# Kernel tuning notes

Measured on AMD Instinct MI355X. Metric: run time of the kernel, lower is better.

The kernel has to match this reference:

```python
import jax, jax.numpy as jnp
import numpy as np

H, D, K, FF = 8, 512, 64, 64  # n_head, feature_dim, key_feature_dim, dim_feedforward
L, B = 512, 32
LN_EPS = 1e-5


def _l2norm(x, eps=1e-12):
    # torch F.normalize: x / max(||x||, eps)
    n = jnp.sqrt(jnp.sum(x * x, axis=-1, keepdims=True))
    return x / jnp.maximum(n, eps)


def _layernorm(x, g, b, eps=LN_EPS):
    m = jnp.mean(x, axis=-1, keepdims=True)
    v = jnp.mean((x - m) ** 2, axis=-1, keepdims=True)
    return (x - m) * jax.lax.rsqrt(v + eps) * g + b


def setup_inputs() -> dict:
    key0 = jax.random.key(0)
    ks = jax.random.split(key0, 13)
    n = jax.random.normal
    s_kq = float(np.sqrt(2.0 / K))
    s_v = float(np.sqrt(2.0 / D))
    return {
        "query": n(ks[0], (L, B, D), jnp.float32),
        "key": n(ks[1], (L, B, D), jnp.float32),
        "value": n(ks[2], (L, B, D), jnp.float32),
        "WK": n(ks[3], (H, K, D), jnp.float32) * s_kq,
        "WQ": n(ks[4], (H, K, D), jnp.float32) * s_kq,
        "WV": n(ks[5], (H, D, D), jnp.float32) * s_v,
        "Wt": n(ks[6], (H, D, D), jnp.float32) * 0.04,  # trans_conv (default kaiming-ish scale)
        "W1": n(ks[7], (H, FF, D), jnp.float32) * 0.04,
        "b1": jnp.zeros((H, FF), jnp.float32),
        "W2": n(ks[8], (H, D, FF), jnp.float32) * 0.1,
        "b2": jnp.zeros((H, D), jnp.float32),
        "ln_g": jnp.ones((H, D), jnp.float32),
        "ln_b": jnp.zeros((H, D), jnp.float32),
    }


def reference(query, key, value, WK, WQ, WV, Wt, W1, b1, W2, b2, ln_g, ln_b):
    # query/key/value: [L, B, D]; per-head weights stacked on leading H axis.
    Lq, Bb, Dd = query.shape
    Hh = WK.shape[0]

    # per-head cosine-normalized Q/K projections: [H, B, L, K]
    wq = _l2norm(jnp.einsum('lbd,hkd->hblk', query, WQ))
    wk = _l2norm(jnp.einsum('lbd,hkd->hblk', key, WK))

    # attention scores [H, B, Lq, Lk], temp = 1
    dot = jnp.einsum('hbqc,hbkc->hbqk', wq, wk)
    aff = jax.nn.softmax(dot, axis=-1)
    # custom renorm: divide by column sums over the QUERY axis
    aff = aff / (1e-9 + jnp.sum(aff, axis=2, keepdims=True))

    wv = jnp.einsum('lbd,hed->hble', value, WV)        # [H, B, Lk, D]
    out = jnp.einsum('hbqk,hbke->hbqe', aff, wv)       # [H, B, Lq, D]
    out = jnp.transpose(out, (0, 2, 1, 3))             # [H, L, B, D]

    # residual-style trans_conv(query - out) -> relu
    o = jax.nn.relu(jnp.einsum('hlbd,hed->hlbe', query[None] - out, Wt))

    # TransNonlinear FFN (dropout = identity at eval)
    hff = jax.nn.relu(jnp.einsum('hlbd,hfd->hlbf', o, W1) + b1[:, None, None, :])
    s2 = jnp.einsum('hlbf,hdf->hlbd', hff, W2) + b2[:, None, None, :]
    x = _layernorm(o + s2, ln_g[:, None, None, :], ln_b[:, None, None, :])

    # concat heads on last dim, head 0 first: [L, B, H*D]
    return jnp.transpose(x, (1, 2, 0, 3)).reshape(Lq, Bb, Hh * Dd)
```

## Files before the change

### kernel.cpp

```cpp
#include <hip/hip_runtime.h>
#include <stdint.h>

#define HH 8
#define DDIM 512
#define KHEAD 64
#define FFD 64
#define LLEN 512
#define BBATCH 32
#define NTOK 16384

typedef unsigned short u16;
typedef __attribute__((ext_vector_type(8))) __bf16 bf16x8;
typedef __attribute__((ext_vector_type(4))) float f32x4;

__device__ __forceinline__ float bf2f(u16 u) {
    union { uint32_t i; float f; } v; v.i = ((uint32_t)u) << 16; return v.f;
}
__device__ __forceinline__ u16 f2bf(float f) {
    union { uint32_t i; float f; } v; v.f = f;
    return (u16)((v.i + 0x7FFFu + ((v.i >> 16) & 1u)) >> 16);
}

__device__ __forceinline__ void gload16(const void* g, void* l) {
    __builtin_amdgcn_global_load_lds(
        (const __attribute__((address_space(1))) void*)g,
        (__attribute__((address_space(3))) void*)l, 16, 0, 0);
}

__global__ __launch_bounds__(256) void f2bf4(const float* __restrict__ in,
                                             u16* __restrict__ out, int n4) {
    int i = blockIdx.x * 256 + threadIdx.x;
    if (i >= n4) return;
    float4 v = ((const float4*)in)[i];
    ushort4 o; o.x = f2bf(v.x); o.y = f2bf(v.y); o.z = f2bf(v.z); o.w = f2bf(v.w);
    ((ushort4*)out)[i] = o;
}

enum { M_PLAIN = 0, M_WQK = 1, M_SUBAUX = 2, M_RELU = 3, M_ADDAUX = 4, M_SCALECOL = 5 };

template<int BM, int BN, int MODE, int ZMAP, int SWAPXY>
__global__ __launch_bounds__(256) void mgemm(
    const u16* __restrict__ A, const u16* __restrict__ B, u16* __restrict__ C,
    int Kd, int lda, int ldb, int ldc,
    long Ash, long Asb, long Bsh, long Bsb, long Csh, long Csb, int nB2,
    const float* __restrict__ bias, int biasN,
    const void* __restrict__ auxp, long auxsh, long auxsb, int auxld)
{
    constexpr int WC = (BN == 128) ? 2 : 1;
    constexpr int WR = 4 / WC;
    constexpr int WTM = BM / WR;
    constexpr int WTN = BN / WC;
    constexpr int MF = WTM / 16;
    constexpr int NF = WTN / 16;
    constexpr int NCA = (BM * 64) / 4096;
    constexpr int NCB = (BN * 64) / 4096;
    __shared__ u16 As[2][BM * 32];
    __shared__ u16 Bs[2][BN * 32];

    const int z = blockIdx.z;
    int h2, b2;
    if (ZMAP == 0)      { h2 = z / nB2;      b2 = z % nB2; }
    else if (ZMAP == 1) { h2 = z & 7;        b2 = z >> 3; }
    else                { h2 = (z >> 3) & 7; b2 = ((z >> 6) << 3) | (z & 7); }
    const u16* Ab = A + h2 * Ash + b2 * Asb;
    const u16* Bb = B + h2 * Bsh + b2 * Bsb;
    const int bx = SWAPXY ? blockIdx.y : blockIdx.x;
    const int by = SWAPXY ? blockIdx.x : blockIdx.y;
    const int m0 = bx * BM, n0 = by * BN;
    const int t = threadIdx.x;
    const int lane = t & 63;
    const int w = t >> 6;
    const int wr = w / WC, wc = w % WC;
    const int tb = t * 16;
    const int wb = (t & 192) * 16;

    f32x4 acc[MF][NF];
    #pragma unroll
    for (int m = 0; m < MF; ++m)
        #pragma unroll
        for (int n = 0; n < NF; ++n)
            #pragma unroll
            for (int i = 0; i < 4; ++i) acc[m][n][i] = 0.f;

    const int ko = (lane >> 4) * 16;

    auto stage = [&](int buf, int k0) {
        #pragma unroll
        for (int c = 0; c < NCA; ++c) {
            const int byte = c * 4096 + tb;
            const int row = byte >> 6;
            gload16((const char*)(Ab + (long)(m0 + row) * lda + k0) + (byte & 63),
                    (char*)As[buf] + c * 4096 + wb);
        }
        #pragma unroll
        for (int c = 0; c < NCB; ++c) {
            const int byte = c * 4096 + tb;
            const int row = byte >> 6;
            gload16((const char*)(Bb + (long)(n0 + row) * ldb + k0) + (byte & 63),
                    (char*)Bs[buf] + c * 4096 + wb);
        }
    };

    stage(0, 0);
    __syncthreads();
    int cur = 0;
    const int nsteps = Kd >> 5;
    for (int s = 0; s < nsteps; ++s) {
        if (s + 1 < nsteps) stage(cur ^ 1, (s + 1) << 5);
        bf16x8 af[MF], bfr[NF];
        #pragma unroll
        for (int m = 0; m < MF; ++m)
            af[m] = *(const bf16x8*)((const char*)As[cur] + (wr * WTM + m * 16 + (lane & 15)) * 64 + ko);
        #pragma unroll
        for (int n = 0; n < NF; ++n)
            bfr[n] = *(const bf16x8*)((const char*)Bs[cur] + (wc * WTN + n * 16 + (lane & 15)) * 64 + ko);
        #pragma unroll
        for (int m = 0; m < MF; ++m)
            #pragma unroll
            for (int n = 0; n < NF; ++n)
                acc[m][n] = __builtin_amdgcn_mfma_f32_16x16x32_bf16(af[m], bfr[n], acc[m][n], 0, 0, 0);
        __syncthreads();
        cur ^= 1;
    }

    const int lr = (lane >> 4) * 4;
    const int lc = lane & 15;

    if constexpr (MODE == M_WQK) {
        const int h = (n0 + wc * WTN) >> 6;
        #pragma unroll
        for (int m = 0; m < MF; ++m) {
            #pragma unroll
            for (int i = 0; i < 4; ++i) {
                float s = 0.f;
                #pragma unroll
                for (int n = 0; n < NF; ++n) { const float v = acc[m][n][i]; s += v * v; }
                s += __shfl_xor(s, 1); s += __shfl_xor(s, 2);
                s += __shfl_xor(s, 4); s += __shfl_xor(s, 8);
                const float inv = 1.0f / fmaxf(sqrtf(s), 1e-12f);
                const int r = m0 + wr * WTM + m * 16 + lr + i;
                const int l = r >> 5, bq = r & 31;
                const int sw = (l & 7) << 3;
                u16* rowp = C + (((long)(h * BBATCH + bq) * LLEN + l) * KHEAD);
                #pragma unroll
                for (int n = 0; n < NF; ++n)
                    rowp[(lc + n * 16) ^ sw] = f2bf(acc[m][n][i] * inv);
            }
        }
    } else {
        const long cof = h2 * Csh + b2 * Csb;
        #pragma unroll
        for (int m = 0; m < MF; ++m) {
            #pragma unroll
            for (int i = 0; i < 4; ++i) {
                const int r = m0 + wr * WTM + m * 16 + lr + i;
                #pragma unroll
                for (int n = 0; n < NF; ++n) {
                    const int c = n0 + wc * WTN + n * 16 + lc;
                    float v = acc[m][n][i];
                    if (MODE == M_SUBAUX) {
                        const u16* q = (const u16*)auxp;
                        v = bf2f(q[auxsh * h2 + auxsb * b2 + (long)r * auxld + c]) - v;
                    } else if (MODE == M_RELU) {
                        if (bias) v += bias[h2 * biasN + c];
                        v = fmaxf(v, 0.0f);
                    } else if (MODE == M_ADDAUX) {
                        v += bias[h2 * biasN + c];
                        const u16* ax = (const u16*)auxp;
                        v += bf2f(ax[auxsh * h2 + auxsb * b2 + (long)r * auxld + c]);
                    } else if (MODE == M_SCALECOL) {
                        const float* cs = (const float*)auxp + auxsh * h2 + auxsb * b2;
                        v *= 1.0f / (1e-9f + cs[c]);
                    }
                    C[cof + (long)r * ldc + c] = f2bf(v);
                }
            }
        }
    }
}

__global__ __launch_bounds__(256) void attn_mfma(
    const u16* __restrict__ wq, const u16* __restrict__ wk,
    u16* __restrict__ P, float* __restrict__ colsum)
{
    __shared__ u16 qs[64 * 64];
    __shared__ u16 ks[512 * 64];
    __shared__ float smax[4][64];
    __shared__ float ssum[4][64];

    const int qt = blockIdx.x, b = blockIdx.y, h = blockIdx.z;
    const long hb = h * BBATCH + b;
    const int t = threadIdx.x;
    const int lane = t & 63, w = t >> 6;
    const int wb = (t & 192) * 16;

    const char* qg = (const char*)(wq + (hb * LLEN + qt * 64) * KHEAD);
    const char* kg = (const char*)(wk + hb * LLEN * KHEAD);
    #pragma unroll
    for (int c = 0; c < 2; ++c)
        gload16(qg + c * 4096 + t * 16, (char*)qs + c * 4096 + wb);
    #pragma unroll
    for (int c = 0; c < 16; ++c)
        gload16(kg + c * 4096 + t * 16, (char*)ks + c * 4096 + wb);
    __syncthreads();

    const int l15 = lane & 15;
    const int g = lane >> 4;
    const int swz = (lane & 7) << 4;

    f32x4 acc[4][8];
    #pragma unroll
    for (int m = 0; m < 4; ++m)
        #pragma unroll
        for (int n = 0; n < 8; ++n)
            #pragma unroll
            for (int i = 0; i < 4; ++i) acc[m][n][i] = 0.f;

    #pragma unroll
    for (int kk = 0; kk < 2; ++kk) {
        bf16x8 af[4];
        #pragma unroll
        for (int m = 0; m < 4; ++m) {
            const int row = m * 16 + l15;
            af[m] = *(const bf16x8*)((const char*)qs + row * 128 + ((g * 16 + kk * 64) ^ swz));
        }
        #pragma unroll
        for (int n = 0; n < 8; ++n) {
            const int row = (w * 8 + n) * 16 + l15;
            const bf16x8 bfr = *(const bf16x8*)((const char*)ks + row * 128 + ((g * 16 + kk * 64) ^ swz));
            #pragma unroll
            for (int m = 0; m < 4; ++m)
                acc[m][n] = __builtin_amdgcn_mfma_f32_16x16x32_bf16(af[m], bfr, acc[m][n], 0, 0, 0);
        }
    }

    float rmax[4][4];
    #pragma unroll
    for (int m = 0; m < 4; ++m)
        #pragma unroll
        for (int i = 0; i < 4; ++i) {
            float mx = acc[m][0][i];
            #pragma unroll
            for (int n = 1; n < 8; ++n) mx = fmaxf(mx, acc[m][n][i]);
            mx = fmaxf(mx, __shfl_xor(mx, 1));
            mx = fmaxf(mx, __shfl_xor(mx, 2));
            mx = fmaxf(mx, __shfl_xor(mx, 4));
            mx = fmaxf(mx, __shfl_xor(mx, 8));
            if (l15 == 0) smax[w][m * 16 + g * 4 + i] = mx;
        }
    __syncthreads();
    #pragma unroll
    for (int m = 0; m < 4; ++m)
        #pragma unroll
        for (int i = 0; i < 4; ++i) {
            const int r = m * 16 + g * 4 + i;
            rmax[m][i] = fmaxf(fmaxf(smax[0][r], smax[1][r]),
                               fmaxf(smax[2][r], smax[3][r]));
        }
    float rinv[4][4];
    #pragma unroll
    for (int m = 0; m < 4; ++m)
        #pragma unroll
        for (int i = 0; i < 4; ++i) {
            float s = 0.f;
            #pragma unroll
            for (int n = 0; n < 8; ++n) {
                acc[m][n][i] = __expf(acc[m][n][i] - rmax[m][i]);
                s += acc[m][n][i];
            }
            s += __shfl_xor(s, 1); s += __shfl_xor(s, 2);
            s += __shfl_xor(s, 4); s += __shfl_xor(s, 8);
            if (l15 == 0) ssum[w][m * 16 + g * 4 + i] = s;
        }
    __syncthreads();
    #pragma unroll
    for (int m = 0; m < 4; ++m)
        #pragma unroll
        for (int i = 0; i < 4; ++i) {
            const int r = m * 16 + g * 4 + i;
            rinv[m][i] = 1.0f / (ssum[0][r] + ssum[1][r] + ssum[2][r] + ssum[3][r]);
        }

    u16* Pb = P + (hb * LLEN + qt * 64) * LLEN + w * 128;
    float cs[8];
    #pragma unroll
    for (int n = 0; n < 8; ++n) cs[n] = 0.f;
    #pragma unroll
    for (int m = 0; m < 4; ++m)
        #pragma unroll
        for (int i = 0; i < 4; ++i) {
            const int r = m * 16 + g * 4 + i;
            u16* pr = Pb + (long)r * LLEN + l15;
            const float iv = rinv[m][i];
            #pragma unroll
            for (int n = 0; n < 8; ++n) {
                const float p = acc[m][n][i] * iv;
                pr[n * 16] = f2bf(p);
                cs[n] += p;
            }
        }
    #pragma unroll
    for (int n = 0; n < 8; ++n) {
        cs[n] += __shfl_xor(cs[n], 16);
        cs[n] += __shfl_xor(cs[n], 32);
    }
    if (lane < 16) {
        float* cb = colsum + hb * 512 + w * 128 + lane;
        #pragma unroll
        for (int n = 0; n < 8; ++n) atomicAdd(&cb[n * 16], cs[n]);
    }
}

__global__ __launch_bounds__(256) void ffn2_ln(
    const u16* __restrict__ hff, const u16* __restrict__ W2bf,
    const float* __restrict__ b2, const u16* __restrict__ o,
    const float* __restrict__ lng, const float* __restrict__ lnb,
    float* __restrict__ out)
{
    __shared__ u16 W2s[512 * 64];
    __shared__ u16 hs[32 * 64];
    __shared__ float redS[4][32];
    __shared__ float redQ[4][32];

    const int h = blockIdx.z;
    const int m0 = blockIdx.x * 32;
    const int t = threadIdx.x;
    const int lane = t & 63, w = t >> 6;
    const int l15 = lane & 15, g = lane >> 4;
    const int wb = (t & 192) * 16;

    const char* w2g = (const char*)W2bf + (long)h * 65536;
    #pragma unroll
    for (int c = 0; c < 16; ++c)
        gload16(w2g + c * 4096 + t * 16, (char*)W2s + c * 4096 + wb);
    gload16((const char*)hff + ((long)h * NTOK + m0) * 128 + t * 16, (char*)hs + wb);
    __syncthreads();

    f32x4 acc[2][8];
    #pragma unroll
    for (int m = 0; m < 2; ++m)
        #pragma unroll
        for (int n = 0; n < 8; ++n)
            #pragma unroll
            for (int i = 0; i < 4; ++i) acc[m][n][i] = 0.f;

    #pragma unroll
    for (int kk = 0; kk < 2; ++kk) {
        bf16x8 af[2];
        #pragma unroll
        for (int m = 0; m < 2; ++m)
            af[m] = *(const bf16x8*)((const char*)hs + (m * 16 + l15) * 128 + kk * 64 + g * 16);
        #pragma unroll
        for (int n = 0; n < 8; ++n) {
            const int e = w * 128 + n * 16 + l15;
            const bf16x8 bfr = *(const bf16x8*)((const char*)W2s + e * 128 + kk * 64 + g * 16);
            #pragma unroll
            for (int m = 0; m < 2; ++m)
                acc[m][n] = __builtin_amdgcn_mfma_f32_16x16x32_bf16(af[m], bfr, acc[m][n], 0, 0, 0);
        }
    }

    float b2v[8], gv[8], bv[8];
    #pragma unroll
    for (int n = 0; n < 8; ++n) {
        const int c = w * 128 + n * 16 + l15;
        b2v[n] = b2[h * DDIM + c];
        gv[n] = lng[h * DDIM + c];
        bv[n] = lnb[h * DDIM + c];
    }
    const u16* ob = o + ((long)h * NTOK + m0) * DDIM;
    #pragma unroll
    for (int m = 0; m < 2; ++m)
        #pragma unroll
        for (int i = 0; i < 4; ++i) {
            const int row = m * 16 + g * 4 + i;
            float s = 0.f, q = 0.f;
            #pragma unroll
            for (int n = 0; n < 8; ++n) {
                const int c = w * 128 + n * 16 + l15;
                const float v = acc[m][n][i] + b2v[n] + bf2f(ob[(long)row * DDIM + c]);
                acc[m][n][i] = v;
                s += v; q += v * v;
            }
            s += __shfl_xor(s, 1); q += __shfl_xor(q, 1);
            s += __shfl_xor(s, 2); q += __shfl_xor(q, 2);
            s += __shfl_xor(s, 4); q += __shfl_xor(q, 4);
            s += __shfl_xor(s, 8); q += __shfl_xor(q, 8);
            if (l15 == 0) { redS[w][row] = s; redQ[w][row] = q; }
        }
    __syncthreads();

    #pragma unroll
    for (int m = 0; m < 2; ++m)
        #pragma unroll
        for (int i = 0; i < 4; ++i) {
            const int row = m * 16 + g * 4 + i;
            const float s = redS[0][row] + redS[1][row] + redS[2][row] + redS[3][row];
            const float q = redQ[0][row] + redQ[1][row] + redQ[2][row] + redQ[3][row];
            const float mu = s * (1.0f / 512.0f);
            const float var = q * (1.0f / 512.0f) - mu * mu;
            const float rs = rsqrtf(var + 1e-5f);
            const int tok = m0 + row;
            const int b = tok >> 9, l = tok & 511;
            float* op = out + ((long)(l * BBATCH + b)) * (HH * DDIM) + h * DDIM;
            #pragma unroll
            for (int n = 0; n < 8; ++n) {
                const int c = w * 128 + n * 16 + l15;
                op[c] = (acc[m][n][i] - mu) * rs * gv[n] + bv[n];
            }
        }
}

extern "C" void kernel_launch(void* const* d_in, const int* in_sizes, int n_in,
                              void* d_out, int out_size, void* d_ws, size_t ws_size,
                              hipStream_t stream) {
    const float* query = (const float*)d_in[0];
    const float* key   = (const float*)d_in[1];
    const float* value = (const float*)d_in[2];
    const float* WK = (const float*)d_in[3];
    const float* WQ = (const float*)d_in[4];
    const float* WV = (const float*)d_in[5];
    const float* Wt = (const float*)d_in[6];
    const float* W1 = (const float*)d_in[7];
    const float* b1 = (const float*)d_in[8];
    const float* W2 = (const float*)d_in[9];
    const float* b2 = (const float*)d_in[10];
    const float* lng = (const float*)d_in[11];
    const float* lnb = (const float*)d_in[12];

    char* ws = (char*)d_ws;
    u16* kbf  = (u16*)(ws);
    u16* WQbf = (u16*)(ws + 16777216);
    u16* WKbf = (u16*)(ws + 17301504);
    u16* P    = (u16*)(ws);
    u16* vbf  = (u16*)(ws + 134217728);
    u16* WVbf = (u16*)(ws + 150994944);
    u16* o    = (u16*)(ws + 134217728);
    float* colsum = (float*)(ws + 268435456);
    u16* qbf  = (u16*)(ws + 268959744);
    u16* hff  = qbf;
    u16* wq   = (u16*)(ws + 285736960);
    u16* wk   = (u16*)(ws + 302514176);
    u16* Wtbf = (u16*)(ws + 285736960);
    u16* W1bf = (u16*)(ws + 289931264);
    u16* W2bf = (u16*)(ws + 290455552);
    u16* qmo = (u16*)d_out;
    u16* wvT = (u16*)((char*)d_out + 134217728);

    if (ws_size < 319291392u) return;

    hipMemsetAsync(colsum, 0, 524288, stream);
    const dim3 blk(256);

    f2bf4<<<dim3(8192), blk, 0, stream>>>(query, qbf, 2097152);
    f2bf4<<<dim3(8192), blk, 0, stream>>>(key,   kbf, 2097152);
    f2bf4<<<dim3(8192), blk, 0, stream>>>(value, vbf, 2097152);
    f2bf4<<<dim3(256),  blk, 0, stream>>>(WQ, WQbf, 65536);
    f2bf4<<<dim3(256),  blk, 0, stream>>>(WK, WKbf, 65536);
    f2bf4<<<dim3(2048), blk, 0, stream>>>(WV, WVbf, 524288);

    mgemm<128, 128, M_WQK, 0, 1><<<dim3(4, 128, 1), blk, 0, stream>>>(
        qbf, WQbf, wq, 512, 512, 512, 0,
        0, 0, 0, 0, 0, 0, 1, nullptr, 0, nullptr, 0, 0, 0);
    mgemm<128, 128, M_WQK, 0, 1><<<dim3(4, 128, 1), blk, 0, stream>>>(
        kbf, WKbf, wk, 512, 512, 512, 0,
        0, 0, 0, 0, 0, 0, 1, nullptr, 0, nullptr, 0, 0, 0);

    attn_mfma<<<dim3(8, 32, 8), blk, 0, stream>>>(wq, wk, P, colsum);

    f2bf4<<<dim3(2048), blk, 0, stream>>>(Wt, Wtbf, 524288);
    f2bf4<<<dim3(256),  blk, 0, stream>>>(W1, W1bf, 65536);
    f2bf4<<<dim3(256),  blk, 0, stream>>>(W2, W2bf, 65536);

    mgemm<128, 128, M_SCALECOL, 2, 0><<<dim3(4, 4, 256), blk, 0, stream>>>(
        WVbf, vbf, wvT, 512, 512, BBATCH * DDIM, 512,
        (long)DDIM * DDIM, 0, 0, DDIM,
        (long)BBATCH * DDIM * LLEN, (long)DDIM * LLEN, 32,
        nullptr, 0, colsum, (long)BBATCH * 512, 512, 0);

    mgemm<128, 128, M_SUBAUX, 1, 0><<<dim3(4, 4, 256), blk, 0, stream>>>(
        P, wvT, qmo, 512, 512, 512, 512,
        (long)BBATCH * LLEN * LLEN, (long)LLEN * LLEN,
        (long)BBATCH * DDIM * LLEN, (long)DDIM * LLEN,
        (long)BBATCH * LLEN * DDIM, (long)LLEN * DDIM, 32,
        nullptr, 0, qbf, 0, DDIM, BBATCH * DDIM);

    mgemm<128, 128, M_RELU, 0, 1><<<dim3(4, 128, 8), blk, 0, stream>>>(
        qmo, Wtbf, o, 512, 512, 512, 512,
        (long)NTOK * DDIM, 0, (long)DDIM * DDIM, 0,
        (long)NTOK * DDIM, 0, 1, nullptr, 512, nullptr, 0, 0, 0);

    mgemm<128, 64, M_RELU, 0, 0><<<dim3(128, 1, 8), blk, 0, stream>>>(
        o, W1bf, hff, 512, 512, 512, 64,
        (long)NTOK * DDIM, 0, (long)FFD * DDIM, 0,
        (long)NTOK * FFD, 0, 1, b1, 64, nullptr, 0, 0, 0);

    ffn2_ln<<<dim3(512, 1, 8), blk, 0, stream>>>(hff, W2bf, b2, o, lng, lnb,
                                                 (float*)d_out);
}
```

Measured before the change: 771.8 us.

## Use conflict-free LDS layouts and explicit vmcnt waits in GEMM pipeline

The generic GEMM now stages tiles into LDS in a k-slot-major layout, so each MFMA fragment read walks contiguous 16-byte rows instead of 64-byte strided rows. This is meant to remove LDS bank conflicts. The double-buffer loop replaces __syncthreads with explicit s_waitcnt vmcnt counts and raw barriers, letting the next tile's global->LDS loads stay in flight while the current tile is computed. The FFN second-layer kernel XOR-swizzles its W2 and hidden tiles in LDS for the same reason. The hand-coded vmcnt values assume a fixed number of loads per stage, which could break if the tile shapes change.

Measured after the change: 943.9 us. +22.3%, slower.

```diff
diff --git a/kernel.cpp b/kernel.cpp
--- a/kernel.cpp
+++ b/kernel.cpp
@@ -25,6 +25,21 @@
     __builtin_amdgcn_global_load_lds(
         (const __attribute__((address_space(1))) void*)g,
         (__attribute__((address_space(3))) void*)l, 16, 0, 0);
+}
+
+template<int R>
+__device__ __forceinline__ void stage_tile(const u16* base, int ld, int k0,
+                                           char* lds, int t) {
+    constexpr int NC = (R * 64) / 4096;
+    const int wb = (t & 192) * 16;
+    #pragma unroll
+    for (int c = 0; c < NC; ++c) {
+        const int idx = c * 4096 + t * 16;
+        const int slot = idx / (R * 16);
+        const int row = (idx >> 4) % R;
+        gload16((const char*)(base + (long)row * ld + k0) + slot * 16,
+                lds + c * 4096 + wb);
+    }
 }
 
 __global__ __launch_bounds__(256) void f2bf4(const float* __restrict__ in,
@@ -52,8 +67,7 @@
     constexpr int WTN = BN / WC;
     constexpr int MF = WTM / 16;
     constexpr int NF = WTN / 16;
-    constexpr int NCA = (BM * 64) / 4096;
-    constexpr int NCB = (BN * 64) / 4096;
+    constexpr int NLD = (BM * 64) / 4096 + (BN * 64) / 4096;
     __shared__ u16 As[2][BM * 32];
     __shared__ u16 Bs[2][BN * 32];
 
@@ -62,17 +76,17 @@
     if (ZMAP == 0)      { h2 = z / nB2;      b2 = z % nB2; }
     else if (ZMAP == 1) { h2 = z & 7;        b2 = z >> 3; }
     else                { h2 = (z >> 3) & 7; b2 = ((z >> 6) << 3) | (z & 7); }
-    const u16* Ab = A + h2 * Ash + b2 * Asb;
-    const u16* Bb = B + h2 * Bsh + b2 * Bsb;
     const int bx = SWAPXY ? blockIdx.y : blockIdx.x;
     const int by = SWAPXY ? blockIdx.x : blockIdx.y;
     const int m0 = bx * BM, n0 = by * BN;
+    const u16* AbM = A + h2 * Ash + b2 * Asb + (long)m0 * lda;
+    const u16* BbN = B + h2 * Bsh + b2 * Bsb + (long)n0 * ldb;
     const int t = threadIdx.x;
     const int lane = t & 63;
     const int w = t >> 6;
     const int wr = w / WC, wc = w % WC;
-    const int tb = t * 16;
-    const int wb = (t & 192) * 16;
+    const int l15 = lane & 15;
+    const int g = lane >> 4;
 
     f32x4 acc[MF][NF];
     #pragma unroll
@@ -82,49 +96,50 @@
             #pragma unroll
             for (int i = 0; i < 4; ++i) acc[m][n][i] = 0.f;
 
-    const int ko = (lane >> 4) * 16;
-
-    auto stage = [&](int buf, int k0) {
-        #pragma unroll
-        for (int c = 0; c < NCA; ++c) {
-            const int byte = c * 4096 + tb;
-            const int row = byte >> 6;
-            gload16((const char*)(Ab + (long)(m0 + row) * lda + k0) + (byte & 63),
-                    (char*)As[buf] + c * 4096 + wb);
-        }
-        #pragma unroll
-        for (int c = 0; c < NCB; ++c) {
-            const int byte = c * 4096 + tb;
-            const int row = byte >> 6;
-            gload16((const char*)(Bb + (long)(n0 + row) * ldb + k0) + (byte & 63),
-                    (char*)Bs[buf] + c * 4096 + wb);
-        }
-    };
-
-    stage(0, 0);
-    __syncthreads();
+    stage_tile<BM>(AbM, lda, 0, (char*)As[0], t);
+    stage_tile<BN>(BbN, ldb, 0, (char*)Bs[0], t);
+
     int cur = 0;
     const int nsteps = Kd >> 5;
     for (int s = 0; s < nsteps; ++s) {
-        if (s + 1 < nsteps) stage(cur ^ 1, (s + 1) << 5);
+        if (s + 1 < nsteps) {
+            stage_tile<BM>(AbM, lda, (s + 1) << 5, (char*)As[cur ^ 1], t);
+            stage_tile<BN>(BbN, ldb, (s + 1) << 5, (char*)Bs[cur ^ 1], t);
+            __builtin_amdgcn_sched_barrier(0);
+            if constexpr (NLD == 4)      asm volatile("s_waitcnt vmcnt(4)" ::: "memory");
+            else if constexpr (NLD == 3) asm volatile("s_waitcnt vmcnt(3)" ::: "memory");
+            else                         asm volatile("s_waitcnt vmcnt(2)" ::: "memory");
+        } else {
+            __builtin_amdgcn_sched_barrier(0);
+            asm volatile("s_waitcnt vmcnt(0)" ::: "memory");
+        }
+        __builtin_amdgcn_sched_barrier(0);
+        __builtin_amdgcn_s_barrier();
+        __builtin_amdgcn_sched_barrier(0);
+
         bf16x8 af[MF], bfr[NF];
         #pragma unroll
         for (int m = 0; m < MF; ++m)
-            af[m] = *(const bf16x8*)((const char*)As[cur] + (wr * WTM + m * 16 + (lane & 15)) * 64 + ko);
+            af[m] = *(const bf16x8*)((const char*)As[cur] + g * (BM * 16) +
+                                     (wr * WTM + m * 16 + l15) * 16);
         #pragma unroll
         for (int n = 0; n < NF; ++n)
-            bfr[n] = *(const bf16x8*)((const char*)Bs[cur] + (wc * WTN + n * 16 + (lane & 15)) * 64 + ko);
+            bfr[n] = *(const bf16x8*)((const char*)Bs[cur] + g * (BN * 16) +
+                                      (wc * WTN + n * 16 + l15) * 16);
         #pragma unroll
         for (int m = 0; m < MF; ++m)
             #pragma unroll
             for (int n = 0; n < NF; ++n)
                 acc[m][n] = __builtin_amdgcn_mfma_f32_16x16x32_bf16(af[m], bfr[n], acc[m][n], 0, 0, 0);
-        __syncthreads();
+
+        __builtin_amdgcn_sched_barrier(0);
+        __builtin_amdgcn_s_barrier();
+        __builtin_amdgcn_sched_barrier(0);
         cur ^= 1;
     }
 
-    const int lr = (lane >> 4) * 4;
-    const int lc = lane & 15;
+    const int lr = g * 4;
+    const int lc = l15;
 
     if constexpr (MODE == M_WQK) {
         const int h = (n0 + wc * WTN) >> 6;
@@ -331,9 +346,21 @@
 
     const char* w2g = (const char*)W2bf + (long)h * 65536;
     #pragma unroll
-    for (int c = 0; c < 16; ++c)
-        gload16(w2g + c * 4096 + t * 16, (char*)W2s + c * 4096 + wb);
-    gload16((const char*)hff + ((long)h * NTOK + m0) * 128 + t * 16, (char*)hs + wb);
+    for (int c = 0; c < 16; ++c) {
+        const int idx = c * 4096 + t * 16;
+        const int row = idx >> 7;
+        const int g0 = (idx >> 4) & 7;
+        gload16(w2g + row * 128 + ((g0 ^ (row & 7)) << 4),
+                (char*)W2s + c * 4096 + wb);
+    }
+    {
+        const int idx = t * 16;
+        const int row = idx >> 7;
+        const int g0 = (idx >> 4) & 7;
+        gload16((const char*)(hff + ((long)h * NTOK + m0) * FFD) +
+                    row * 128 + ((g0 ^ (row & 7)) << 4),
+                (char*)hs + wb);
+    }
     __syncthreads();
 
     f32x4 acc[2][8];
@@ -348,12 +375,16 @@
     for (int kk = 0; kk < 2; ++kk) {
         bf16x8 af[2];
         #pragma unroll
-        for (int m = 0; m < 2; ++m)
-            af[m] = *(const bf16x8*)((const char*)hs + (m * 16 + l15) * 128 + kk * 64 + g * 16);
+        for (int m = 0; m < 2; ++m) {
+            const int row = m * 16 + l15;
+            af[m] = *(const bf16x8*)((const char*)hs + row * 128 +
+                                     (((kk * 4 + g) ^ (row & 7)) << 4));
+        }
         #pragma unroll
         for (int n = 0; n < 8; ++n) {
             const int e = w * 128 + n * 16 + l15;
-            const bf16x8 bfr = *(const bf16x8*)((const char*)W2s + e * 128 + kk * 64 + g * 16);
+            const bf16x8 bfr = *(const bf16x8*)((const char*)W2s + e * 128 +
+                                                (((kk * 4 + g) ^ (e & 7)) << 4));
             #pragma unroll
             for (int m = 0; m < 2; ++m)
                 acc[m][n] = __builtin_amdgcn_mfma_f32_16x16x32_bf16(af[m], bfr, acc[m][n], 0, 0, 0);
```

## Fuse softmax with PV product, recompute attention instead of materializing P

Applied to the files above, without the earlier changes.

Attention probabilities are no longer written to a large bf16 P buffer. A first kernel computes only the softmax column sums. A new fused kernel recomputes QK^T and the softmax, stores P in swizzled LDS, and multiplies it by the column-scaled V with double-buffered staging, writing query minus output directly. This removes the P write and read traffic at the cost of computing QK^T twice. The change also adds an XOR swizzle to the LDS layout in ffn2_ln and moves the weight conversions earlier, placing those buffers at new workspace offsets.

Measured after the change: 844.1 us. 1.09x slower.

```diff
diff --git a/kernel.cpp b/kernel.cpp
--- a/kernel.cpp
+++ b/kernel.cpp
@@ -179,9 +179,9 @@
     }
 }
 
-__global__ __launch_bounds__(256) void attn_mfma(
+__global__ __launch_bounds__(256) void attn_sums(
     const u16* __restrict__ wq, const u16* __restrict__ wk,
-    u16* __restrict__ P, float* __restrict__ colsum)
+    float* __restrict__ colsum)
 {
     __shared__ u16 qs[64 * 64];
     __shared__ u16 ks[512 * 64];
@@ -281,7 +281,6 @@
             rinv[m][i] = 1.0f / (ssum[0][r] + ssum[1][r] + ssum[2][r] + ssum[3][r]);
         }
 
-    u16* Pb = P + (hb * LLEN + qt * 64) * LLEN + w * 128;
     float cs[8];
     #pragma unroll
     for (int n = 0; n < 8; ++n) cs[n] = 0.f;
@@ -289,15 +288,9 @@
     for (int m = 0; m < 4; ++m)
         #pragma unroll
         for (int i = 0; i < 4; ++i) {
-            const int r = m * 16 + g * 4 + i;
-            u16* pr = Pb + (long)r * LLEN + l15;
             const float iv = rinv[m][i];
             #pragma unroll
-            for (int n = 0; n < 8; ++n) {
-                const float p = acc[m][n][i] * iv;
-                pr[n * 16] = f2bf(p);
-                cs[n] += p;
-            }
+            for (int n = 0; n < 8; ++n) cs[n] += acc[m][n][i] * iv;
         }
     #pragma unroll
     for (int n = 0; n < 8; ++n) {
@@ -309,6 +302,184 @@
         #pragma unroll
         for (int n = 0; n < 8; ++n) atomicAdd(&cb[n * 16], cs[n]);
     }
+}
+
+__global__ __launch_bounds__(512) void attn_pv(
+    const u16* __restrict__ wq, const u16* __restrict__ wk,
+    const u16* __restrict__ wvT, const u16* __restrict__ qbf,
+    u16* __restrict__ qmo)
+{
+    __shared__ u16 ksP[512 * 64];
+    __shared__ u16 stg[2][512 * 32];
+    __shared__ float smax[8][64];
+    __shared__ float ssum[8][64];
+
+    const int qt = blockIdx.x, b = blockIdx.y, h = blockIdx.z;
+    const long hb = h * BBATCH + b;
+    const int t = threadIdx.x;
+    const int lane = t & 63, w = t >> 6;
+    const int l15 = lane & 15, g = lane >> 4;
+    const int wb = (t & 448) * 16;
+
+    const char* qg = (const char*)(wq + (hb * LLEN + qt * 64) * KHEAD);
+    const char* kg = (const char*)(wk + hb * LLEN * KHEAD);
+    gload16(qg + t * 16, (char*)stg + wb);
+    #pragma unroll
+    for (int c = 0; c < 8; ++c)
+        gload16(kg + c * 8192 + t * 16, (char*)ksP + c * 8192 + wb);
+    __syncthreads();
+
+    const int swz = (l15 & 7) << 4;
+
+    f32x4 acc[4][4];
+    #pragma unroll
+    for (int m = 0; m < 4; ++m)
+        #pragma unroll
+        for (int n = 0; n < 4; ++n)
+            #pragma unroll
+            for (int i = 0; i < 4; ++i) acc[m][n][i] = 0.f;
+
+    #pragma unroll
+    for (int kk = 0; kk < 2; ++kk) {
+        bf16x8 af[4];
+        #pragma unroll
+        for (int m = 0; m < 4; ++m) {
+            const int row = m * 16 + l15;
+            af[m] = *(const bf16x8*)((const char*)stg + row * 128 + ((g * 16 + kk * 64) ^ swz));
+        }
+        #pragma unroll
+        for (int n = 0; n < 4; ++n) {
+            const int row = w * 64 + n * 16 + l15;
+            const bf16x8 bfr = *(const bf16x8*)((const char*)ksP + row * 128 + ((g * 16 + kk * 64) ^ swz));
+            #pragma unroll
+            for (int m = 0; m < 4; ++m)
+                acc[m][n] = __builtin_amdgcn_mfma_f32_16x16x32_bf16(af[m], bfr, acc[m][n], 0, 0, 0);
+        }
+    }
+
+    #pragma unroll
+    for (int m = 0; m < 4; ++m)
+        #pragma unroll
+        for (int i = 0; i < 4; ++i) {
+            float mx = acc[m][0][i];
+            #pragma unroll
+            for (int n = 1; n < 4; ++n) mx = fmaxf(mx, acc[m][n][i]);
+            mx = fmaxf(mx, __shfl_xor(mx, 1));
+            mx = fmaxf(mx, __shfl_xor(mx, 2));
+            mx = fmaxf(mx, __shfl_xor(mx, 4));
+            mx = fmaxf(mx, __shfl_xor(mx, 8));
+            if (l15 == 0) smax[w][m * 16 + g * 4 + i] = mx;
+        }
+    __syncthreads();
+    float rmax[4][4];
+    #pragma unroll
+    for (int m = 0; m < 4; ++m)
+        #pragma unroll
+        for (int i = 0; i < 4; ++i) {
+            const int r = m * 16 + g * 4 + i;
+            float mx = smax[0][r];
+            #pragma unroll
+            for (int ww = 1; ww < 8; ++ww) mx = fmaxf(mx, smax[ww][r]);
+            rmax[m][i] = mx;
+        }
+    #pragma unroll
+    for (int m = 0; m < 4; ++m)
+        #pragma unroll
+        for (int i = 0; i < 4; ++i) {
+            float s = 0.f;
+            #pragma unroll
+            for (int n = 0; n < 4; ++n) {
+                acc[m][n][i] = __expf(acc[m][n][i] - rmax[m][i]);
+                s += acc[m][n][i];
+            }
+            s += __shfl_xor(s, 1); s += __shfl_xor(s, 2);
+            s += __shfl_xor(s, 4); s += __shfl_xor(s, 8);
+            if (l15 == 0) ssum[w][m * 16 + g * 4 + i] = s;
+        }
+    __syncthreads();
+    float rinv[4][4];
+    #pragma unroll
+    for (int m = 0; m < 4; ++m)
+        #pragma unroll
+        for (int i = 0; i < 4; ++i) {
+            const int r = m * 16 + g * 4 + i;
+            float s = ssum[0][r];
+            #pragma unroll
+            for (int ww = 1; ww < 8; ++ww) s += ssum[ww][r];
+            rinv[m][i] = 1.0f / s;
+        }
+
+    const u16* wvb = wvT + hb * (long)DDIM * LLEN;
+    auto stgv = [&](int buf, int s) {
+        #pragma unroll
+        for (int c = 0; c < 4; ++c) {
+            const int byte = c * 8192 + t * 16;
+            const int row = byte >> 6;
+            gload16((const char*)wvb + (long)row * 1024 + s * 64 + (byte & 63),
+                    (char*)stg[buf] + c * 8192 + wb);
+        }
+    };
+    stgv(0, 0);
+
+    #pragma unroll
+    for (int m = 0; m < 4; ++m)
+        #pragma unroll
+        for (int i = 0; i < 4; ++i) {
+            const int q = m * 16 + g * 4 + i;
+            const float iv = rinv[m][i];
+            #pragma unroll
+            for (int n = 0; n < 4; ++n) {
+                const int k = w * 64 + n * 16 + l15;
+                const int Gs = (k >> 3) ^ (q & 7);
+                *(u16*)((char*)ksP + q * 1024 + Gs * 16 + (k & 7) * 2) =
+                    f2bf(acc[m][n][i] * iv);
+            }
+        }
+    __syncthreads();
+
+    f32x4 o[4][4];
+    #pragma unroll
+    for (int m = 0; m < 4; ++m)
+        #pragma unroll
+        for (int n = 0; n < 4; ++n)
+            #pragma unroll
+            for (int i = 0; i < 4; ++i) o[m][n][i] = 0.f;
+
+    int cur = 0;
+    for (int s = 0; s < 16; ++s) {
+        if (s + 1 < 16) stgv(cur ^ 1, s + 1);
+        bf16x8 pa[4];
+        #pragma unroll
+        for (int m = 0; m < 4; ++m) {
+            const int q = m * 16 + l15;
+            pa[m] = *(const bf16x8*)((const char*)ksP + q * 1024 +
+                                     (((s * 4 + g) ^ (q & 7)) << 4));
+        }
+        #pragma unroll
+        for (int n = 0; n < 4; ++n) {
+            const int row = w * 64 + n * 16 + l15;
+            const bf16x8 vb = *(const bf16x8*)((const char*)stg[cur] + row * 64 + g * 16);
+            #pragma unroll
+            for (int m = 0; m < 4; ++m)
+                o[m][n] = __builtin_amdgcn_mfma_f32_16x16x32_bf16(pa[m], vb, o[m][n], 0, 0, 0);
+        }
+        __syncthreads();
+        cur ^= 1;
+    }
+
+    #pragma unroll
+    for (int m = 0; m < 4; ++m)
+        #pragma unroll
+        for (int i = 0; i < 4; ++i) {
+            const int q = qt * 64 + m * 16 + g * 4 + i;
+            const u16* qrow = qbf + ((long)q * BBATCH + b) * DDIM;
+            u16* orow = qmo + (hb * LLEN + q) * DDIM;
+            #pragma unroll
+            for (int n = 0; n < 4; ++n) {
+                const int e = w * 64 + n * 16 + l15;
+                orow[e] = f2bf(bf2f(qrow[e]) - o[m][n][i]);
+            }
+        }
 }
 
 __global__ __launch_bounds__(256) void ffn2_ln(
@@ -331,9 +502,21 @@
 
     const char* w2g = (const char*)W2bf + (long)h * 65536;
     #pragma unroll
-    for (int c = 0; c < 16; ++c)
-        gload16(w2g + c * 4096 + t * 16, (char*)W2s + c * 4096 + wb);
-    gload16((const char*)hff + ((long)h * NTOK + m0) * 128 + t * 16, (char*)hs + wb);
+    for (int c = 0; c < 16; ++c) {
+        const int idx = c * 4096 + t * 16;
+        const int row = idx >> 7;
+        const int g0 = (idx >> 4) & 7;
+        gload16(w2g + row * 128 + ((g0 ^ (row & 7)) << 4),
+                (char*)W2s + c * 4096 + wb);
+    }
+    {
+        const int idx = t * 16;
+        const int row = idx >> 7;
+        const int g0 = (idx >> 4) & 7;
+        gload16((const char*)(hff + ((long)h * NTOK + m0) * FFD) +
+                    row * 128 + ((g0 ^ (row & 7)) << 4),
+                (char*)hs + wb);
+    }
     __syncthreads();
 
     f32x4 acc[2][8];
@@ -348,12 +531,16 @@
     for (int kk = 0; kk < 2; ++kk) {
         bf16x8 af[2];
         #pragma unroll
-        for (int m = 0; m < 2; ++m)
-            af[m] = *(const bf16x8*)((const char*)hs + (m * 16 + l15) * 128 + kk * 64 + g * 16);
+        for (int m = 0; m < 2; ++m) {
+            const int row = m * 16 + l15;
+            af[m] = *(const bf16x8*)((const char*)hs + row * 128 +
+                                     (((kk * 4 + g) ^ (row & 7)) << 4));
+        }
         #pragma unroll
         for (int n = 0; n < 8; ++n) {
             const int e = w * 128 + n * 16 + l15;
-            const bf16x8 bfr = *(const bf16x8*)((const char*)W2s + e * 128 + kk * 64 + g * 16);
+            const bf16x8 bfr = *(const bf16x8*)((const char*)W2s + e * 128 +
+                                                (((kk * 4 + g) ^ (e & 7)) << 4));
             #pragma unroll
             for (int m = 0; m < 2; ++m)
                 acc[m][n] = __builtin_amdgcn_mfma_f32_16x16x32_bf16(af[m], bfr, acc[m][n], 0, 0, 0);
@@ -432,7 +619,9 @@
     u16* kbf  = (u16*)(ws);
     u16* WQbf = (u16*)(ws + 16777216);
     u16* WKbf = (u16*)(ws + 17301504);
-    u16* P    = (u16*)(ws);
+    u16* Wtbf = (u16*)(ws + 33554432);
+    u16* W1bf = (u16*)(ws + 37748736);
+    u16* W2bf = (u16*)(ws + 38273024);
     u16* vbf  = (u16*)(ws + 134217728);
     u16* WVbf = (u16*)(ws + 150994944);
     u16* o    = (u16*)(ws + 134217728);
@@ -441,9 +630,6 @@
     u16* hff  = qbf;
     u16* wq   = (u16*)(ws + 285736960);
     u16* wk   = (u16*)(ws + 302514176);
-    u16* Wtbf = (u16*)(ws + 285736960);
-    u16* W1bf = (u16*)(ws + 289931264);
-    u16* W2bf = (u16*)(ws + 290455552);
     u16* qmo = (u16*)d_out;
     u16* wvT = (u16*)((char*)d_out + 134217728);
 
@@ -458,6 +644,9 @@
     f2bf4<<<dim3(256),  blk, 0, stream>>>(WQ, WQbf, 65536);
     f2bf4<<<dim3(256),  blk, 0, stream>>>(WK, WKbf, 65536);
     f2bf4<<<dim3(2048), blk, 0, stream>>>(WV, WVbf, 524288);
+    f2bf4<<<dim3(2048), blk, 0, stream>>>(Wt, Wtbf, 524288);
+    f2bf4<<<dim3(256),  blk, 0, stream>>>(W1, W1bf, 65536);
+    f2bf4<<<dim3(256),  blk, 0, stream>>>(W2, W2bf, 65536);
 
     mgemm<128, 128, M_WQK, 0, 1><<<dim3(4, 128, 1), blk, 0, stream>>>(
         qbf, WQbf, wq, 512, 512, 512, 0,
@@ -466,11 +655,7 @@
         kbf, WKbf, wk, 512, 512, 512, 0,
         0, 0, 0, 0, 0, 0, 1, nullptr, 0, nullptr, 0, 0, 0);
 
-    attn_mfma<<<dim3(8, 32, 8), blk, 0, stream>>>(wq, wk, P, colsum);
-
-    f2bf4<<<dim3(2048), blk, 0, stream>>>(Wt, Wtbf, 524288);
-    f2bf4<<<dim3(256),  blk, 0, stream>>>(W1, W1bf, 65536);
-    f2bf4<<<dim3(256),  blk, 0, stream>>>(W2, W2bf, 65536);
+    attn_sums<<<dim3(8, 32, 8), blk, 0, stream>>>(wq, wk, colsum);
 
     mgemm<128, 128, M_SCALECOL, 2, 0><<<dim3(4, 4, 256), blk, 0, stream>>>(
         WVbf, vbf, wvT, 512, 512, BBATCH * DDIM, 512,
@@ -478,12 +663,7 @@
         (long)BBATCH * DDIM * LLEN, (long)DDIM * LLEN, 32,
         nullptr, 0, colsum, (long)BBATCH * 512, 512, 0);
 
-    mgemm<128, 128, M_SUBAUX, 1, 0><<<dim3(4, 4, 256), blk, 0, stream>>>(
-        P, wvT, qmo, 512, 512, 512, 512,
-        (long)BBATCH * LLEN * LLEN, (long)LLEN * LLEN,
-        (long)BBATCH * DDIM * LLEN, (long)DDIM * LLEN,
-        (long)BBATCH * LLEN * DDIM, (long)LLEN * DDIM, 32,
-        nullptr, 0, qbf, 0, DDIM, BBATCH * DDIM);
+    attn_pv<<<dim3(8, 32, 8), dim3(512), 0, stream>>>(wq, wk, wvT, qbf, qmo);
 
     mgemm<128, 128, M_RELU, 0, 1><<<dim3(4, 128, 8), blk, 0, stream>>>(
         qmo, Wtbf, o, 512, 512, 512, 512,
```
